# Kernel tuning notes

Hardware: AMD Instinct MI355X
Metric: run time of the kernel (lower is better)

## Reference

```python
import jax, jax.numpy as jnp
import numpy as np

N_HEADS = 16
D_HEAD = 64
N_ROTATE = 32
ROPE_BASE = 10000.0
MAX_LEN = 2048  # round_up_to_multiple_of_256(keep count); static for jit
BATCH, SEQ = 2, 4096


def setup_inputs() -> dict:
    key = jax.random.key(0)
    kq, kk, kv = jax.random.split(key, 3)
    q = jax.random.normal(kq, (BATCH, N_HEADS, MAX_LEN, D_HEAD), jnp.float32)
    k = jax.random.normal(kk, (BATCH, N_HEADS, SEQ, D_HEAD), jnp.float32)
    v = jax.random.normal(kv, (BATCH, N_HEADS, SEQ, D_HEAD), jnp.float32)
    # causal full mask [batch, seq, seq] and full position ids [batch, seq]
    mask_full = jnp.broadcast_to(jnp.tril(jnp.ones((SEQ, SEQ), bool)), (BATCH, SEQ, SEQ))
    pos_full = jnp.broadcast_to(jnp.arange(SEQ, dtype=jnp.int32), (BATCH, SEQ))
    # skip_mask: exactly MAX_LEN kept tokens per row (random positions)
    rng = np.random.default_rng(0)
    sm = np.zeros((BATCH, SEQ), dtype=bool)
    for i in range(BATCH):
        sm[i, rng.permutation(SEQ)[:MAX_LEN]] = True
    return {"q": q, "k": k, "v": v, "mask_full": mask_full,
            "pos_full": pos_full, "skip_mask": jnp.asarray(sm)}


def _rope_rotate(x, pos):
    # x: [b, h, L, n_rotate], pos: [b, L]
    half = N_ROTATE // 2
    inv_freq = 1.0 / (ROPE_BASE ** (jnp.arange(0, N_ROTATE, 2, dtype=jnp.float32) / N_ROTATE))
    freqs = pos.astype(jnp.float32)[..., None] * inv_freq          # [b, L, half]
    emb = jnp.concatenate([freqs, freqs], axis=-1)[:, None]        # [b, 1, L, n_rotate]
    cos, sin = jnp.cos(emb), jnp.sin(emb)
    x1, x2 = x[..., :half], x[..., half:]
    rot = jnp.concatenate([-x2, x1], axis=-1)                      # rotate_half
    return x * cos + rot * sin


def reference(q, k, v, mask_full, pos_full, skip_mask):
    b, S = skip_mask.shape
    lengths = skip_mask.sum(axis=1)
    # vectorized _trim_attention_mask: stable argsort compacts kept indices to the front
    order = jnp.argsort(jnp.where(skip_mask, 0, 1), axis=1, stable=True)
    idx = order[:, :MAX_LEN]                                       # [b, max_len]
    brow = jnp.arange(b)[:, None]
    mask_trim = mask_full[brow, idx]                               # [b, max_len, S]
    pos_trim = pos_full[brow, idx]                                 # [b, max_len]
    valid = jnp.arange(MAX_LEN)[None, :] < lengths[:, None]
    mask_trim = mask_trim & valid[..., None]
    pos_trim = jnp.where(valid, pos_trim, 0)

    # partial RoPE on first n_rotate channels
    rq = _rope_rotate(q[..., :N_ROTATE], pos_trim)
    rk = _rope_rotate(k[..., :N_ROTATE], pos_full)
    q = jnp.concatenate([rq, q[..., N_ROTATE:]], axis=-1)
    k = jnp.concatenate([rk, k[..., N_ROTATE:]], axis=-1)

    # masked SDPA (bool mask broadcast over heads)
    scale = 1.0 / jnp.sqrt(jnp.float32(D_HEAD))
    scores = jnp.einsum('bhqd,bhkd->bhqk', q, k) * scale
    scores = jnp.where(mask_trim[:, None], scores, jnp.finfo(scores.dtype).min)
    attn = jax.nn.softmax(scores, axis=-1)
    return jnp.einsum('bhqk,bhkd->bhqd', attn, v)
```

## Files before the change

kernel.cpp:

```cpp
#include <hip/hip_runtime.h>
#include <math.h>

#define BB 2
#define HH 16
#define QQ 2048
#define SS 4096
#define DD 64
#define NRH 16
#define NQT 32

typedef unsigned short u16;
typedef unsigned int   u32;
typedef short bhalf8 __attribute__((ext_vector_type(8)));
typedef float f32x4  __attribute__((ext_vector_type(4)));

typedef __attribute__((address_space(1))) const u32 gu32;
typedef __attribute__((address_space(3))) u32 lu32;

#if __has_builtin(__builtin_amdgcn_exp2f)
#define EXP2(x) __builtin_amdgcn_exp2f(x)
#else
#define EXP2(x) exp2f(x)
#endif

union Frag16 { uint4 u; bhalf8 v; u16 s[8]; uint2 d[2]; };

__device__ __forceinline__ u16 f2bf(float f) {
  union { float f; u32 u; } c; c.f = f;
  return (u16)((c.u + 0x7FFFu + ((c.u >> 16) & 1u)) >> 16);
}

__device__ __forceinline__ u32 cvt_pk_bf16(float lo, float hi) {
  u32 r;
  asm("v_cvt_pk_bf16_f32 %0, %1, %2" : "=v"(r) : "v"(lo), "v"(hi));
  return r;
}

__device__ __forceinline__ bhalf8 ldfrag(const u16* p) {
  Frag16 f; f.u = *reinterpret_cast<const uint4*>(p); return f.v;
}

__device__ __forceinline__ void rope32(float* x, int pos) {
  const float step = 0.8304820237218405f;
  const float fp = (float)pos;
#pragma unroll
  for (int i = 0; i < NRH; ++i) {
    float ang = fp * exp2f(-step * (float)i);
    float sv, cv;
    __sincosf(ang, &sv, &cv);
    float a = x[i], b = x[i + NRH];
    x[i]       = a * cv - b * sv;
    x[i + NRH] = b * cv + a * sv;
  }
}

__global__ void prep_idx_kernel(const unsigned char* __restrict__ sm,
                                int* __restrict__ idx) {
  __shared__ int wsum[4];
  __shared__ int modes;
  const int tid = threadIdx.x;
  const int b = (int)blockIdx.x;

  int c = 0;
  for (int i = 0; i < 32; ++i) c += (sm[tid * 32 + i] != 0) ? 1 : 0;
#pragma unroll
  for (int off = 32; off; off >>= 1) c += __shfl_down(c, off);
  if ((tid & 63) == 0) wsum[tid >> 6] = c;
  __syncthreads();
  if (tid == 0) modes = (wsum[0] + wsum[1] + wsum[2] + wsum[3] > 3000) ? 1 : 0;
  __syncthreads();
  const bool byteMode = (modes != 0);
  const u32* sm32 = (const u32*)sm;

  const int base = b * SS + tid * 16;
  u32 flags = 0;
  for (int i = 0; i < 16; ++i) {
    bool f = byteMode ? (sm[base + i] != 0) : (sm32[base + i] != 0);
    flags |= ((u32)(f ? 1 : 0)) << i;
  }
  int cnt = __popc(flags);
  int vv = cnt;
#pragma unroll
  for (int off = 1; off < 64; off <<= 1) {
    int t = __shfl_up(vv, off);
    if ((tid & 63) >= off) vv += t;
  }
  __syncthreads();
  if ((tid & 63) == 63) wsum[tid >> 6] = vv;
  __syncthreads();
  int add = 0;
  for (int w2 = 0; w2 < (tid >> 6); ++w2) add += wsum[w2];
  int p = vv - cnt + add;
  for (int i = 0; i < 16; ++i) {
    if (flags & (1u << i)) {
      if (p < QQ) idx[b * QQ + p] = tid * 16 + i;
      ++p;
    }
  }
}

__global__ __launch_bounds__(256) void prep_kv_kernel(const float* __restrict__ k,
                                                      const float* __restrict__ v,
                                                      u16* __restrict__ kbf,
                                                      u16* __restrict__ vt) {
  __shared__ u16 tile[64][72];
  if (blockIdx.x < 512) {
    int r = blockIdx.x * 256 + threadIdx.x;
    int pos = r & (SS - 1);
    float x[64];
    const float4* src = (const float4*)(k + (size_t)r * DD);
#pragma unroll
    for (int i = 0; i < 16; ++i) {
      float4 t = src[i];
      x[4 * i] = t.x; x[4 * i + 1] = t.y; x[4 * i + 2] = t.z; x[4 * i + 3] = t.w;
    }
    rope32(x, pos);
    u16 tmp[64];
#pragma unroll
    for (int i = 0; i < 64; ++i) tmp[i] = f2bf(x[i]);
    uint4* dst = (uint4*)(kbf + (size_t)r * DD);
#pragma unroll
    for (int i = 0; i < 8; ++i) dst[i] = ((uint4*)tmp)[i];
  } else {
    int blk = (int)blockIdx.x - 512;
    int bh = blk >> 6;
    int jt = blk & 63;
    int t = threadIdx.x;
    int jl = t >> 2;
    int dc = (t & 3) * 16;
    const float4* src = (const float4*)(v + ((size_t)(bh * SS + jt * 64 + jl)) * DD + dc);
#pragma unroll
    for (int i = 0; i < 4; ++i) {
      float4 f = src[i];
      tile[jl][dc + 4 * i]     = f2bf(f.x);
      tile[jl][dc + 4 * i + 1] = f2bf(f.y);
      tile[jl][dc + 4 * i + 2] = f2bf(f.z);
      tile[jl][dc + 4 * i + 3] = f2bf(f.w);
    }
    __syncthreads();
    int d = t >> 2;
    int c = t & 3;
    u16 o[16];
#pragma unroll
    for (int m = 0; m < 16; ++m)
      o[m] = tile[4 * c + (m >> 2) + ((m & 3) << 4)][d];
    uint4* dst = (uint4*)(vt + ((size_t)(bh * DD + d)) * SS + jt * 64 + c * 16);
    dst[0] = ((uint4*)o)[0];
    dst[1] = ((uint4*)o)[1];
  }
}

__device__ __forceinline__ void stage_tiles(const char* kb_bh, const char* vt_bh,
                                            u16* Kb, u16* Vb, int t0,
                                            int w, int srow, int schk) {
#pragma unroll
  for (int p2 = 0; p2 < 2; ++p2) {
    const int rr = w * 16 + p2 * 8 + srow;
    {
      const char* g = kb_bh + (size_t)(t0 + rr) * 128 + ((schk ^ (rr & 7)) * 16);
      lu32* l = (lu32*)((char*)Kb + (w * 16 + p2 * 8) * 128);
      __builtin_amdgcn_global_load_lds((gu32*)g, l, 16, 0, 0);
    }
    {
      const char* g = vt_bh + (size_t)rr * (SS * 2) + t0 * 2 + ((schk ^ (rr & 7)) * 16);
      lu32* l = (lu32*)((char*)Vb + (w * 16 + p2 * 8) * 128);
      __builtin_amdgcn_global_load_lds((gu32*)g, l, 16, 0, 0);
    }
  }
}

template <bool MASKED>
__device__ __forceinline__ void attn_tile(
    const u16* __restrict__ Kb, const u16* __restrict__ Vb, u16* __restrict__ pb,
    int t0, int grp, int col,
    int bnd0, int bnd1, int bnd2, int bnd3,
    int paIdx0, int paIdx1,
    int pwIdx0, int pwIdx1, int pwIdx2, int pwIdx3,
    bhalf8 qa0, bhalf8 qa1,
    f32x4& acc0, f32x4& acc1, f32x4& acc2, f32x4& acc3,
    float& l0, float& l1, float& l2, float& l3) {
  const int swz = col & 7;
  f32x4 s0 = {0.f, 0.f, 0.f, 0.f}, s1 = s0, s2 = s0, s3 = s0;
  {
    const u16* kr0 = Kb + (0 * 16 + col) * 64;
    const u16* kr1 = Kb + (1 * 16 + col) * 64;
    const u16* kr2 = Kb + (2 * 16 + col) * 64;
    const u16* kr3 = Kb + (3 * 16 + col) * 64;
    __builtin_amdgcn_s_setprio(1);
    s0 = __builtin_amdgcn_mfma_f32_16x16x32_bf16(qa0, ldfrag(kr0 + ((grp ^ swz) * 8)), s0, 0, 0, 0);
    s1 = __builtin_amdgcn_mfma_f32_16x16x32_bf16(qa0, ldfrag(kr1 + ((grp ^ swz) * 8)), s1, 0, 0, 0);
    s2 = __builtin_amdgcn_mfma_f32_16x16x32_bf16(qa0, ldfrag(kr2 + ((grp ^ swz) * 8)), s2, 0, 0, 0);
    s3 = __builtin_amdgcn_mfma_f32_16x16x32_bf16(qa0, ldfrag(kr3 + ((grp ^ swz) * 8)), s3, 0, 0, 0);
    s0 = __builtin_amdgcn_mfma_f32_16x16x32_bf16(qa1, ldfrag(kr0 + (((4 + grp) ^ swz) * 8)), s0, 0, 0, 0);
    s1 = __builtin_amdgcn_mfma_f32_16x16x32_bf16(qa1, ldfrag(kr1 + (((4 + grp) ^ swz) * 8)), s1, 0, 0, 0);
    s2 = __builtin_amdgcn_mfma_f32_16x16x32_bf16(qa1, ldfrag(kr2 + (((4 + grp) ^ swz) * 8)), s2, 0, 0, 0);
    s3 = __builtin_amdgcn_mfma_f32_16x16x32_bf16(qa1, ldfrag(kr3 + (((4 + grp) ^ swz) * 8)), s3, 0, 0, 0);
    __builtin_amdgcn_s_setprio(0);
  }

  const int key0 = t0 + col;
#define SM_ROW(R, BND, LACC, PWI)                                              \
  {                                                                            \
    float p0, p1, p2v, p3;                                                     \
    if (MASKED) {                                                              \
      p0  = (key0      <= (BND)) ? EXP2(s0[R] - 16.f) : 0.f;                   \
      p1  = (key0 + 16 <= (BND)) ? EXP2(s1[R] - 16.f) : 0.f;                   \
      p2v = (key0 + 32 <= (BND)) ? EXP2(s2[R] - 16.f) : 0.f;                   \
      p3  = (key0 + 48 <= (BND)) ? EXP2(s3[R] - 16.f) : 0.f;                   \
    } else {                                                                   \
      p0  = EXP2(s0[R] - 16.f);                                                \
      p1  = EXP2(s1[R] - 16.f);                                                \
      p2v = EXP2(s2[R] - 16.f);                                                \
      p3  = EXP2(s3[R] - 16.f);                                                \
    }                                                                          \
    (LACC) += (p0 + p1) + (p2v + p3);                                          \
    uint2 pw;                                                                  \
    pw.x = cvt_pk_bf16(p0, p1);                                                \
    pw.y = cvt_pk_bf16(p2v, p3);                                               \
    *(uint2*)(pb + (PWI)) = pw;                                                \
  }
  SM_ROW(0, bnd0, l0, pwIdx0)
  SM_ROW(1, bnd1, l1, pwIdx1)
  SM_ROW(2, bnd2, l2, pwIdx2)
  SM_ROW(3, bnd3, l3, pwIdx3)
#undef SM_ROW

  bhalf8 pa0, pa1;
  {
    Frag16 f0, f1;
    f0.u = *(const uint4*)(pb + paIdx0);
    f1.u = *(const uint4*)(pb + paIdx1);
    pa0 = f0.v; pa1 = f1.v;
  }

  {
    const u16* vr0 = Vb + (0 * 16 + col) * 64;
    const u16* vr1 = Vb + (1 * 16 + col) * 64;
    const u16* vr2 = Vb + (2 * 16 + col) * 64;
    const u16* vr3 = Vb + (3 * 16 + col) * 64;
    __builtin_amdgcn_s_setprio(1);
    acc0 = __builtin_amdgcn_mfma_f32_16x16x32_bf16(pa0, ldfrag(vr0 + ((grp ^ swz) * 8)), acc0, 0, 0, 0);
    acc1 = __builtin_amdgcn_mfma_f32_16x16x32_bf16(pa0, ldfrag(vr1 + ((grp ^ swz) * 8)), acc1, 0, 0, 0);
    acc2 = __builtin_amdgcn_mfma_f32_16x16x32_bf16(pa0, ldfrag(vr2 + ((grp ^ swz) * 8)), acc2, 0, 0, 0);
    acc3 = __builtin_amdgcn_mfma_f32_16x16x32_bf16(pa0, ldfrag(vr3 + ((grp ^ swz) * 8)), acc3, 0, 0, 0);
    acc0 = __builtin_amdgcn_mfma_f32_16x16x32_bf16(pa1, ldfrag(vr0 + (((4 + grp) ^ swz) * 8)), acc0, 0, 0, 0);
    acc1 = __builtin_amdgcn_mfma_f32_16x16x32_bf16(pa1, ldfrag(vr1 + (((4 + grp) ^ swz) * 8)), acc1, 0, 0, 0);
    acc2 = __builtin_amdgcn_mfma_f32_16x16x32_bf16(pa1, ldfrag(vr2 + (((4 + grp) ^ swz) * 8)), acc2, 0, 0, 0);
    acc3 = __builtin_amdgcn_mfma_f32_16x16x32_bf16(pa1, ldfrag(vr3 + (((4 + grp) ^ swz) * 8)), acc3, 0, 0, 0);
    __builtin_amdgcn_s_setprio(0);
  }
}

__global__ __launch_bounds__(256, 4) void attn_mfma_kernel(
    const float* __restrict__ qsrc, const u16* __restrict__ kbf,
    const u16* __restrict__ vt, const int* __restrict__ idx,
    float* __restrict__ out) {
  __shared__ u16 KbufA[64 * 64];
  __shared__ u16 VbufA[64 * 64];
  __shared__ u16 KbufB[64 * 64];
  __shared__ u16 VbufB[64 * 64];
  __shared__ __align__(16) u16 Pbuf[4][16 * 64];

  const int blk = (int)blockIdx.x;
  const int bh  = blk & 31;
  const int qt  = (NQT - 1) - (blk >> 5);
  const int q0  = qt * 64;
  const int b   = bh >> 4;
  const int tid  = threadIdx.x;
  const int w    = tid >> 6;
  const int lane = tid & 63;
  const int grp  = lane >> 4;
  const int col  = lane & 15;

  const char* kb_bh = (const char*)(kbf + (size_t)bh * SS * DD);
  const char* vt_bh = (const char*)(vt + (size_t)bh * DD * SS);

  const int srow = lane >> 3;
  const int schk = lane & 7;

  u16* pb = Pbuf[w];

  const int* idxb = idx + b * QQ + q0;
  const int bnd0 = idxb[w * 16 + grp * 4 + 0];
  const int bnd1 = idxb[w * 16 + grp * 4 + 1];
  const int bnd2 = idxb[w * 16 + grp * 4 + 2];
  const int bnd3 = idxb[w * 16 + grp * 4 + 3];
  const int wave_minb = idxb[w * 16];
  const int wave_maxb = idxb[w * 16 + 15];
  const int maxbound  = idxb[63];
  const int ntiles = (maxbound >> 6) + 1;

  const int paIdx0 = col * 64 + ((grp ^ (col & 7)) << 3);
  const int paIdx1 = col * 64 + (((grp + 4) ^ (col & 7)) << 3);
  const int qg = grp * 4;
  const int pwIdx0 = (qg + 0) * 64 + ((((col >> 1) ^ ((qg + 0) & 7))) << 3) + ((col & 1) << 2);
  const int pwIdx1 = (qg + 1) * 64 + ((((col >> 1) ^ ((qg + 1) & 7))) << 3) + ((col & 1) << 2);
  const int pwIdx2 = (qg + 2) * 64 + ((((col >> 1) ^ ((qg + 2) & 7))) << 3) + ((col & 1) << 2);
  const int pwIdx3 = (qg + 3) * 64 + ((((col >> 1) ^ ((qg + 3) & 7))) << 3) + ((col & 1) << 2);

  bhalf8 qa0, qa1;
  {
    const int qrow = q0 + w * 16 + col;
    const int mypos = idx[b * QQ + qrow];
    const float* qr = qsrc + (size_t)(bh * QQ + qrow) * DD;
    const int lof = (grp & 1) * 8;
    float4 A0 = *(const float4*)(qr + lof);
    float4 A1 = *(const float4*)(qr + lof + 4);
    float4 B0 = *(const float4*)(qr + 16 + lof);
    float4 B1 = *(const float4*)(qr + 16 + lof + 4);
    float4 C0 = *(const float4*)(qr + 32 + grp * 8);
    float4 C1 = *(const float4*)(qr + 32 + grp * 8 + 4);
    float xlo[8] = {A0.x, A0.y, A0.z, A0.w, A1.x, A1.y, A1.z, A1.w};
    float xhi[8] = {B0.x, B0.y, B0.z, B0.w, B1.x, B1.y, B1.z, B1.w};
    float xq1[8] = {C0.x, C0.y, C0.z, C0.w, C1.x, C1.y, C1.z, C1.w};
    const float scq = 0.125f * 1.44269504088896f;
    const float fp = (float)mypos;
    Frag16 f0, f1;
#pragma unroll
    for (int j = 0; j < 8; ++j) {
      float ang = fp * exp2f(-0.8304820237218405f * (float)(lof + j));
      float sv, cv;
      __sincosf(ang, &sv, &cv);
      float val = (grp >= 2) ? (xhi[j] * cv + xlo[j] * sv)
                             : (xlo[j] * cv - xhi[j] * sv);
      f0.s[j] = f2bf(val * scq);
      f1.s[j] = f2bf(xq1[j] * scq);
    }
    qa0 = f0.v; qa1 = f1.v;
  }

  f32x4 acc0 = {0.f, 0.f, 0.f, 0.f}, acc1 = acc0, acc2 = acc0, acc3 = acc0;
  float l0 = 0.f, l1 = 0.f, l2 = 0.f, l3 = 0.f;

  stage_tiles(kb_bh, vt_bh, KbufA, VbufA, 0, w, srow, schk);
  __syncthreads();

  for (int ti = 0; ti < ntiles; ti += 2) {
    const bool has1 = (ti + 1) < ntiles;
    if (has1) stage_tiles(kb_bh, vt_bh, KbufB, VbufB, (ti + 1) << 6, w, srow, schk);
    {
      const int t0 = ti << 6;
      if (t0 <= wave_maxb) {
        if (t0 + 63 <= wave_minb)
          attn_tile<false>(KbufA, VbufA, pb, t0, grp, col, bnd0, bnd1, bnd2, bnd3,
                           paIdx0, paIdx1, pwIdx0, pwIdx1, pwIdx2, pwIdx3,
                           qa0, qa1, acc0, acc1, acc2, acc3, l0, l1, l2, l3);
        else
          attn_tile<true>(KbufA, VbufA, pb, t0, grp, col, bnd0, bnd1, bnd2, bnd3,
                          paIdx0, paIdx1, pwIdx0, pwIdx1, pwIdx2, pwIdx3,
                          qa0, qa1, acc0, acc1, acc2, acc3, l0, l1, l2, l3);
      }
    }
    __syncthreads();
    if (has1) {
      if (ti + 2 < ntiles)
        stage_tiles(kb_bh, vt_bh, KbufA, VbufA, (ti + 2) << 6, w, srow, schk);
      {
        const int t0 = (ti + 1) << 6;
        if (t0 <= wave_maxb) {
          if (t0 + 63 <= wave_minb)
            attn_tile<false>(KbufB, VbufB, pb, t0, grp, col, bnd0, bnd1, bnd2, bnd3,
                             paIdx0, paIdx1, pwIdx0, pwIdx1, pwIdx2, pwIdx3,
                             qa0, qa1, acc0, acc1, acc2, acc3, l0, l1, l2, l3);
          else
            attn_tile<true>(KbufB, VbufB, pb, t0, grp, col, bnd0, bnd1, bnd2, bnd3,
                            paIdx0, paIdx1, pwIdx0, pwIdx1, pwIdx2, pwIdx3,
                            qa0, qa1, acc0, acc1, acc2, acc3, l0, l1, l2, l3);
        }
      }
      __syncthreads();
    }
  }

#pragma unroll
  for (int mdel = 1; mdel < 16; mdel <<= 1) {
    l0 += __shfl_xor(l0, mdel);
    l1 += __shfl_xor(l1, mdel);
    l2 += __shfl_xor(l2, mdel);
    l3 += __shfl_xor(l3, mdel);
  }
  float i0 = 1.f / l0, i1 = 1.f / l1, i2 = 1.f / l2, i3 = 1.f / l3;
  float* ob = out + (size_t)(bh * QQ + q0 + w * 16 + grp * 4) * DD + col;
#pragma unroll
  for (int r = 0; r < 4; ++r) {
    float iv = (r == 0) ? i0 : (r == 1) ? i1 : (r == 2) ? i2 : i3;
    ob[(size_t)r * DD + 0]  = acc0[r] * iv;
    ob[(size_t)r * DD + 16] = acc1[r] * iv;
    ob[(size_t)r * DD + 32] = acc2[r] * iv;
    ob[(size_t)r * DD + 48] = acc3[r] * iv;
  }
}

__global__ __launch_bounds__(64) void attn_fb_kernel(const float* __restrict__ q,
                                                     const float* __restrict__ ksrc,
                                                     const float* __restrict__ v,
                                                     const int* __restrict__ idx,
                                                     float* __restrict__ out) {
  int t = (int)(gridDim.x - 1u - blockIdx.x);
  int sub = t >> 5;
  int bh = t & 31;
  int b = bh >> 4;
  int lane = threadIdx.x;
  int qi = sub * 64 + lane;
  const int bound = idx[b * QQ + qi];

  float qreg[64];
  {
    const float4* qp = (const float4*)(q + ((size_t)bh * QQ + qi) * DD);
#pragma unroll
    for (int i = 0; i < 16; ++i) {
      float4 t4 = qp[i];
      qreg[4 * i] = t4.x; qreg[4 * i + 1] = t4.y;
      qreg[4 * i + 2] = t4.z; qreg[4 * i + 3] = t4.w;
    }
  }
  rope32(qreg, bound);
#pragma unroll
  for (int i = 0; i < 64; ++i) qreg[i] *= 0.125f;

  const float* kbase = ksrc + (size_t)bh * SS * DD;
  const float* vbase = v + (size_t)bh * SS * DD;
  float acc[64];
#pragma unroll
  for (int i = 0; i < 64; ++i) acc[i] = 0.f;
  float mrun = -INFINITY, lrun = 0.f;

  for (int j = 0; j <= bound; ++j) {
    float ka[64];
    const float4* kp = (const float4*)(kbase + (size_t)j * DD);
#pragma unroll
    for (int i = 0; i < 16; ++i) {
      float4 t4 = kp[i];
      ka[4 * i] = t4.x; ka[4 * i + 1] = t4.y;
      ka[4 * i + 2] = t4.z; ka[4 * i + 3] = t4.w;
    }
    rope32(ka, j);
    float s0 = 0.f, s1 = 0.f, s2 = 0.f, s3 = 0.f;
#pragma unroll
    for (int i = 0; i < 16; ++i) {
      s0 = fmaf(qreg[4 * i], ka[4 * i], s0);
      s1 = fmaf(qreg[4 * i + 1], ka[4 * i + 1], s1);
      s2 = fmaf(qreg[4 * i + 2], ka[4 * i + 2], s2);
      s3 = fmaf(qreg[4 * i + 3], ka[4 * i + 3], s3);
    }
    float sc = (s0 + s1) + (s2 + s3);
    if (sc > mrun) {
      float alpha = __expf(mrun - sc);
      lrun *= alpha;
#pragma unroll
      for (int i = 0; i < 64; ++i) acc[i] *= alpha;
      mrun = sc;
    }
    float pw = __expf(sc - mrun);
    lrun += pw;
    const float4* vp = (const float4*)(vbase + (size_t)j * DD);
#pragma unroll
    for (int i = 0; i < 16; ++i) {
      float4 t4 = vp[i];
      acc[4 * i] = fmaf(pw, t4.x, acc[4 * i]);
      acc[4 * i + 1] = fmaf(pw, t4.y, acc[4 * i + 1]);
      acc[4 * i + 2] = fmaf(pw, t4.z, acc[4 * i + 2]);
      acc[4 * i + 3] = fmaf(pw, t4.w, acc[4 * i + 3]);
    }
  }
  float inv = 1.0f / lrun;
  float4* op = (float4*)(out + ((size_t)bh * QQ + qi) * DD);
#pragma unroll
  for (int i = 0; i < 16; ++i) {
    float4 t4;
    t4.x = acc[4 * i] * inv; t4.y = acc[4 * i + 1] * inv;
    t4.z = acc[4 * i + 2] * inv; t4.w = acc[4 * i + 3] * inv;
    op[i] = t4;
  }
}

extern "C" void kernel_launch(void* const* d_in, const int* in_sizes, int n_in,
                              void* d_out, int out_size, void* d_ws, size_t ws_size,
                              hipStream_t stream) {
  (void)in_sizes; (void)n_in; (void)out_size;
  const float* q = (const float*)d_in[0];
  const float* k = (const float*)d_in[1];
  const float* v = (const float*)d_in[2];
  const unsigned char* skip = (const unsigned char*)d_in[5];
  float* out = (float*)d_out;

  char* base = (char*)d_ws;
  int* idx = (int*)base;
  const size_t kbytes = (size_t)BB * HH * SS * DD * 2;
  u16* kbf = (u16*)(base + 16384);
  u16* vtb = (u16*)(base + 16384 + kbytes);
  const size_t need = 16384 + 2 * kbytes;

  prep_idx_kernel<<<2, 256, 0, stream>>>(skip, idx);
  if (ws_size >= need) {
    prep_kv_kernel<<<512 + BB * HH * 64, 256, 0, stream>>>(k, v, kbf, vtb);
    attn_mfma_kernel<<<NQT * 32, 256, 0, stream>>>(q, kbf, vtb, idx, out);
  } else {
    attn_fb_kernel<<<1024, 64, 0, stream>>>(q, k, v, idx, out);
  }
}
```

Before: 296.8 us.

## Compute transposed S and O tiles to keep P in registers, dropping LDS round-trip

Swaps the MFMA operand order so each lane holds scores for one query row across four consecutive keys. The bf16 P fragment can then be packed straight from registers into the PV MFMA operand instead of being written to and read back from a per-wave shared-memory buffer. The V transpose kernel permutes key order to match the new fragment layout. The row-sum reduction shrinks to two shuffles, the mask bound becomes a single per-lane value, and output stores become float4 writes. The risk is that any mismatch between the permuted V layout and the P register packing gives silently wrong results.

```diff
diff --git a/kernel.cpp b/kernel.cpp
--- a/kernel.cpp
+++ b/kernel.cpp
@@ -142,8 +142,11 @@
     int c = t & 3;
     u16 o[16];
 #pragma unroll
-    for (int m = 0; m < 16; ++m)
-      o[m] = tile[4 * c + (m >> 2) + ((m & 3) << 4)][d];
+    for (int m = 0; m < 16; ++m) {
+      int p = c * 16 + m;
+      int kp = (p & 32) | ((p & 4) << 2) | ((p >> 1) & 12) | (p & 3);
+      o[m] = tile[kp][d];
+    }
     uint4* dst = (uint4*)(vt + ((size_t)(bh * DD + d)) * SS + jt * 64 + c * 16);
     dst[0] = ((uint4*)o)[0];
     dst[1] = ((uint4*)o)[1];
@@ -171,82 +174,95 @@
 
 template <bool MASKED>
 __device__ __forceinline__ void attn_tile(
-    const u16* __restrict__ Kb, const u16* __restrict__ Vb, u16* __restrict__ pb,
-    int t0, int grp, int col,
-    int bnd0, int bnd1, int bnd2, int bnd3,
-    int paIdx0, int paIdx1,
-    int pwIdx0, int pwIdx1, int pwIdx2, int pwIdx3,
+    const u16* __restrict__ Kb, const u16* __restrict__ Vb,
+    int t0, int grp, int col, int bnd,
     bhalf8 qa0, bhalf8 qa1,
     f32x4& acc0, f32x4& acc1, f32x4& acc2, f32x4& acc3,
-    float& l0, float& l1, float& l2, float& l3) {
+    float& lsum) {
   const int swz = col & 7;
-  f32x4 s0 = {0.f, 0.f, 0.f, 0.f}, s1 = s0, s2 = s0, s3 = s0;
+  f32x4 z = {0.f, 0.f, 0.f, 0.f};
+  f32x4 s0 = z, s1 = z, s2 = z, s3 = z;
   {
     const u16* kr0 = Kb + (0 * 16 + col) * 64;
     const u16* kr1 = Kb + (1 * 16 + col) * 64;
     const u16* kr2 = Kb + (2 * 16 + col) * 64;
     const u16* kr3 = Kb + (3 * 16 + col) * 64;
     __builtin_amdgcn_s_setprio(1);
-    s0 = __builtin_amdgcn_mfma_f32_16x16x32_bf16(qa0, ldfrag(kr0 + ((grp ^ swz) * 8)), s0, 0, 0, 0);
-    s1 = __builtin_amdgcn_mfma_f32_16x16x32_bf16(qa0, ldfrag(kr1 + ((grp ^ swz) * 8)), s1, 0, 0, 0);
-    s2 = __builtin_amdgcn_mfma_f32_16x16x32_bf16(qa0, ldfrag(kr2 + ((grp ^ swz) * 8)), s2, 0, 0, 0);
-    s3 = __builtin_amdgcn_mfma_f32_16x16x32_bf16(qa0, ldfrag(kr3 + ((grp ^ swz) * 8)), s3, 0, 0, 0);
-    s0 = __builtin_amdgcn_mfma_f32_16x16x32_bf16(qa1, ldfrag(kr0 + (((4 + grp) ^ swz) * 8)), s0, 0, 0, 0);
-    s1 = __builtin_amdgcn_mfma_f32_16x16x32_bf16(qa1, ldfrag(kr1 + (((4 + grp) ^ swz) * 8)), s1, 0, 0, 0);
-    s2 = __builtin_amdgcn_mfma_f32_16x16x32_bf16(qa1, ldfrag(kr2 + (((4 + grp) ^ swz) * 8)), s2, 0, 0, 0);
-    s3 = __builtin_amdgcn_mfma_f32_16x16x32_bf16(qa1, ldfrag(kr3 + (((4 + grp) ^ swz) * 8)), s3, 0, 0, 0);
+    bhalf8 a0 = ldfrag(kr0 + ((grp ^ swz) * 8));
+    s0 = __builtin_amdgcn_mfma_f32_16x16x32_bf16(a0, qa0, s0, 0, 0, 0);
+    bhalf8 b0 = ldfrag(kr0 + (((4 + grp) ^ swz) * 8));
+    s0 = __builtin_amdgcn_mfma_f32_16x16x32_bf16(b0, qa1, s0, 0, 0, 0);
+    bhalf8 a1 = ldfrag(kr1 + ((grp ^ swz) * 8));
+    s1 = __builtin_amdgcn_mfma_f32_16x16x32_bf16(a1, qa0, s1, 0, 0, 0);
+    bhalf8 b1 = ldfrag(kr1 + (((4 + grp) ^ swz) * 8));
+    s1 = __builtin_amdgcn_mfma_f32_16x16x32_bf16(b1, qa1, s1, 0, 0, 0);
+    bhalf8 a2 = ldfrag(kr2 + ((grp ^ swz) * 8));
+    s2 = __builtin_amdgcn_mfma_f32_16x16x32_bf16(a2, qa0, s2, 0, 0, 0);
+    bhalf8 b2 = ldfrag(kr2 + (((4 + grp) ^ swz) * 8));
+    s2 = __builtin_amdgcn_mfma_f32_16x16x32_bf16(b2, qa1, s2, 0, 0, 0);
+    bhalf8 a3 = ldfrag(kr3 + ((grp ^ swz) * 8));
+    s3 = __builtin_amdgcn_mfma_f32_16x16x32_bf16(a3, qa0, s3, 0, 0, 0);
+    bhalf8 b3 = ldfrag(kr3 + (((4 + grp) ^ swz) * 8));
+    s3 = __builtin_amdgcn_mfma_f32_16x16x32_bf16(b3, qa1, s3, 0, 0, 0);
     __builtin_amdgcn_s_setprio(0);
   }
 
-  const int key0 = t0 + col;
-#define SM_ROW(R, BND, LACC, PWI)                                              \
+  uint2 w0, w1, w2, w3;
+#define SM_C(SC, CB, W)                                                        \
   {                                                                            \
     float p0, p1, p2v, p3;                                                     \
+    const int kb = t0 + (CB) + grp * 4;                                        \
     if (MASKED) {                                                              \
-      p0  = (key0      <= (BND)) ? EXP2(s0[R] - 16.f) : 0.f;                   \
-      p1  = (key0 + 16 <= (BND)) ? EXP2(s1[R] - 16.f) : 0.f;                   \
-      p2v = (key0 + 32 <= (BND)) ? EXP2(s2[R] - 16.f) : 0.f;                   \
-      p3  = (key0 + 48 <= (BND)) ? EXP2(s3[R] - 16.f) : 0.f;                   \
+      p0  = (kb + 0 <= bnd) ? EXP2(SC[0] - 16.f) : 0.f;                        \
+      p1  = (kb + 1 <= bnd) ? EXP2(SC[1] - 16.f) : 0.f;                        \
+      p2v = (kb + 2 <= bnd) ? EXP2(SC[2] - 16.f) : 0.f;                        \
+      p3  = (kb + 3 <= bnd) ? EXP2(SC[3] - 16.f) : 0.f;                        \
     } else {                                                                   \
-      p0  = EXP2(s0[R] - 16.f);                                                \
-      p1  = EXP2(s1[R] - 16.f);                                                \
-      p2v = EXP2(s2[R] - 16.f);                                                \
-      p3  = EXP2(s3[R] - 16.f);                                                \
+      p0  = EXP2(SC[0] - 16.f);                                                \
+      p1  = EXP2(SC[1] - 16.f);                                                \
+      p2v = EXP2(SC[2] - 16.f);                                                \
+      p3  = EXP2(SC[3] - 16.f);                                                \
     }                                                                          \
-    (LACC) += (p0 + p1) + (p2v + p3);                                          \
-    uint2 pw;                                                                  \
-    pw.x = cvt_pk_bf16(p0, p1);                                                \
-    pw.y = cvt_pk_bf16(p2v, p3);                                               \
-    *(uint2*)(pb + (PWI)) = pw;                                                \
-  }
-  SM_ROW(0, bnd0, l0, pwIdx0)
-  SM_ROW(1, bnd1, l1, pwIdx1)
-  SM_ROW(2, bnd2, l2, pwIdx2)
-  SM_ROW(3, bnd3, l3, pwIdx3)
-#undef SM_ROW
-
-  bhalf8 pa0, pa1;
+    lsum += (p0 + p1) + (p2v + p3);                                            \
+    W.x = cvt_pk_bf16(p0, p1);                                                 \
+    W.y = cvt_pk_bf16(p2v, p3);                                                \
+  }
+  SM_C(s0, 0,  w0)
+  SM_C(s1, 16, w1)
+  SM_C(s2, 32, w2)
+  SM_C(s3, 48, w3)
+#undef SM_C
+
+  bhalf8 pv0, pv1;
   {
     Frag16 f0, f1;
-    f0.u = *(const uint4*)(pb + paIdx0);
-    f1.u = *(const uint4*)(pb + paIdx1);
-    pa0 = f0.v; pa1 = f1.v;
-  }
-
-  {
-    const u16* vr0 = Vb + (0 * 16 + col) * 64;
-    const u16* vr1 = Vb + (1 * 16 + col) * 64;
-    const u16* vr2 = Vb + (2 * 16 + col) * 64;
-    const u16* vr3 = Vb + (3 * 16 + col) * 64;
+    f0.d[0] = w0; f0.d[1] = w1;
+    f1.d[0] = w2; f1.d[1] = w3;
+    pv0 = f0.v; pv1 = f1.v;
+  }
+
+  {
+    const u16* vr0 = Vb + (0  + col) * 64;
+    const u16* vr1 = Vb + (16 + col) * 64;
+    const u16* vr2 = Vb + (32 + col) * 64;
+    const u16* vr3 = Vb + (48 + col) * 64;
     __builtin_amdgcn_s_setprio(1);
-    acc0 = __builtin_amdgcn_mfma_f32_16x16x32_bf16(pa0, ldfrag(vr0 + ((grp ^ swz) * 8)), acc0, 0, 0, 0);
-    acc1 = __builtin_amdgcn_mfma_f32_16x16x32_bf16(pa0, ldfrag(vr1 + ((grp ^ swz) * 8)), acc1, 0, 0, 0);
-    acc2 = __builtin_amdgcn_mfma_f32_16x16x32_bf16(pa0, ldfrag(vr2 + ((grp ^ swz) * 8)), acc2, 0, 0, 0);
-    acc3 = __builtin_amdgcn_mfma_f32_16x16x32_bf16(pa0, ldfrag(vr3 + ((grp ^ swz) * 8)), acc3, 0, 0, 0);
-    acc0 = __builtin_amdgcn_mfma_f32_16x16x32_bf16(pa1, ldfrag(vr0 + (((4 + grp) ^ swz) * 8)), acc0, 0, 0, 0);
-    acc1 = __builtin_amdgcn_mfma_f32_16x16x32_bf16(pa1, ldfrag(vr1 + (((4 + grp) ^ swz) * 8)), acc1, 0, 0, 0);
-    acc2 = __builtin_amdgcn_mfma_f32_16x16x32_bf16(pa1, ldfrag(vr2 + (((4 + grp) ^ swz) * 8)), acc2, 0, 0, 0);
-    acc3 = __builtin_amdgcn_mfma_f32_16x16x32_bf16(pa1, ldfrag(vr3 + (((4 + grp) ^ swz) * 8)), acc3, 0, 0, 0);
+    bhalf8 x0 = ldfrag(vr0 + ((grp ^ swz) * 8));
+    acc0 = __builtin_amdgcn_mfma_f32_16x16x32_bf16(x0, pv0, acc0, 0, 0, 0);
+    bhalf8 y0 = ldfrag(vr0 + (((4 + grp) ^ swz) * 8));
+    acc0 = __builtin_amdgcn_mfma_f32_16x16x32_bf16(y0, pv1, acc0, 0, 0, 0);
+    bhalf8 x1 = ldfrag(vr1 + ((grp ^ swz) * 8));
+    acc1 = __builtin_amdgcn_mfma_f32_16x16x32_bf16(x1, pv0, acc1, 0, 0, 0);
+    bhalf8 y1 = ldfrag(vr1 + (((4 + grp) ^ swz) * 8));
+    acc1 = __builtin_amdgcn_mfma_f32_16x16x32_bf16(y1, pv1, acc1, 0, 0, 0);
+    bhalf8 x2 = ldfrag(vr2 + ((grp ^ swz) * 8));
+    acc2 = __builtin_amdgcn_mfma_f32_16x16x32_bf16(x2, pv0, acc2, 0, 0, 0);
+    bhalf8 y2 = ldfrag(vr2 + (((4 + grp) ^ swz) * 8));
+    acc2 = __builtin_amdgcn_mfma_f32_16x16x32_bf16(y2, pv1, acc2, 0, 0, 0);
+    bhalf8 x3 = ldfrag(vr3 + ((grp ^ swz) * 8));
+    acc3 = __builtin_amdgcn_mfma_f32_16x16x32_bf16(x3, pv0, acc3, 0, 0, 0);
+    bhalf8 y3 = ldfrag(vr3 + (((4 + grp) ^ swz) * 8));
+    acc3 = __builtin_amdgcn_mfma_f32_16x16x32_bf16(y3, pv1, acc3, 0, 0, 0);
     __builtin_amdgcn_s_setprio(0);
   }
 }
@@ -259,7 +275,6 @@
   __shared__ u16 VbufA[64 * 64];
   __shared__ u16 KbufB[64 * 64];
   __shared__ u16 VbufB[64 * 64];
-  __shared__ __align__(16) u16 Pbuf[4][16 * 64];
 
   const int blk = (int)blockIdx.x;
   const int bh  = blk & 31;
@@ -278,30 +293,16 @@
   const int srow = lane >> 3;
   const int schk = lane & 7;
 
-  u16* pb = Pbuf[w];
-
   const int* idxb = idx + b * QQ + q0;
-  const int bnd0 = idxb[w * 16 + grp * 4 + 0];
-  const int bnd1 = idxb[w * 16 + grp * 4 + 1];
-  const int bnd2 = idxb[w * 16 + grp * 4 + 2];
-  const int bnd3 = idxb[w * 16 + grp * 4 + 3];
+  const int bnd = idxb[w * 16 + col];
   const int wave_minb = idxb[w * 16];
   const int wave_maxb = idxb[w * 16 + 15];
   const int maxbound  = idxb[63];
   const int ntiles = (maxbound >> 6) + 1;
 
-  const int paIdx0 = col * 64 + ((grp ^ (col & 7)) << 3);
-  const int paIdx1 = col * 64 + (((grp + 4) ^ (col & 7)) << 3);
-  const int qg = grp * 4;
-  const int pwIdx0 = (qg + 0) * 64 + ((((col >> 1) ^ ((qg + 0) & 7))) << 3) + ((col & 1) << 2);
-  const int pwIdx1 = (qg + 1) * 64 + ((((col >> 1) ^ ((qg + 1) & 7))) << 3) + ((col & 1) << 2);
-  const int pwIdx2 = (qg + 2) * 64 + ((((col >> 1) ^ ((qg + 2) & 7))) << 3) + ((col & 1) << 2);
-  const int pwIdx3 = (qg + 3) * 64 + ((((col >> 1) ^ ((qg + 3) & 7))) << 3) + ((col & 1) << 2);
-
   bhalf8 qa0, qa1;
   {
     const int qrow = q0 + w * 16 + col;
-    const int mypos = idx[b * QQ + qrow];
     const float* qr = qsrc + (size_t)(bh * QQ + qrow) * DD;
     const int lof = (grp & 1) * 8;
     float4 A0 = *(const float4*)(qr + lof);
@@ -314,7 +315,7 @@
     float xhi[8] = {B0.x, B0.y, B0.z, B0.w, B1.x, B1.y, B1.z, B1.w};
     float xq1[8] = {C0.x, C0.y, C0.z, C0.w, C1.x, C1.y, C1.z, C1.w};
     const float scq = 0.125f * 1.44269504088896f;
-    const float fp = (float)mypos;
+    const float fp = (float)bnd;
     Frag16 f0, f1;
 #pragma unroll
     for (int j = 0; j < 8; ++j) {
@@ -329,8 +330,12 @@
     qa0 = f0.v; qa1 = f1.v;
   }
 
-  f32x4 acc0 = {0.f, 0.f, 0.f, 0.f}, acc1 = acc0, acc2 = acc0, acc3 = acc0;
-  float l0 = 0.f, l1 = 0.f, l2 = 0.f, l3 = 0.f;
+  f32x4 z = {0.f, 0.f, 0.f, 0.f};
+  f32x4 acc0 = z, acc1 = z, acc2 = z, acc3 = z;
+  float lsum = 0.f;
+
+#define ATTN_CALL(M, KB, VB, T0)                                               \
+  attn_tile<M>(KB, VB, T0, grp, col, bnd, qa0, qa1, acc0, acc1, acc2, acc3, lsum)
 
   stage_tiles(kb_bh, vt_bh, KbufA, VbufA, 0, w, srow, schk);
   __syncthreads();
@@ -341,14 +346,8 @@
     {
       const int t0 = ti << 6;
       if (t0 <= wave_maxb) {
-        if (t0 + 63 <= wave_minb)
-          attn_tile<false>(KbufA, VbufA, pb, t0, grp, col, bnd0, bnd1, bnd2, bnd3,
-                           paIdx0, paIdx1, pwIdx0, pwIdx1, pwIdx2, pwIdx3,
-                           qa0, qa1, acc0, acc1, acc2, acc3, l0, l1, l2, l3);
-        else
-          attn_tile<true>(KbufA, VbufA, pb, t0, grp, col, bnd0, bnd1, bnd2, bnd3,
-                          paIdx0, paIdx1, pwIdx0, pwIdx1, pwIdx2, pwIdx3,
-                          qa0, qa1, acc0, acc1, acc2, acc3, l0, l1, l2, l3);
+        if (t0 + 63 <= wave_minb) ATTN_CALL(false, KbufA, VbufA, t0);
+        else                      ATTN_CALL(true,  KbufA, VbufA, t0);
       }
     }
     __syncthreads();
@@ -358,36 +357,29 @@
       {
         const int t0 = (ti + 1) << 6;
         if (t0 <= wave_maxb) {
-          if (t0 + 63 <= wave_minb)
-            attn_tile<false>(KbufB, VbufB, pb, t0, grp, col, bnd0, bnd1, bnd2, bnd3,
-                             paIdx0, paIdx1, pwIdx0, pwIdx1, pwIdx2, pwIdx3,
-                             qa0, qa1, acc0, acc1, acc2, acc3, l0, l1, l2, l3);
-          else
-            attn_tile<true>(KbufB, VbufB, pb, t0, grp, col, bnd0, bnd1, bnd2, bnd3,
-                            paIdx0, paIdx1, pwIdx0, pwIdx1, pwIdx2, pwIdx3,
-                            qa0, qa1, acc0, acc1, acc2, acc3, l0, l1, l2, l3);
+          if (t0 + 63 <= wave_minb) ATTN_CALL(false, KbufB, VbufB, t0);
+          else                      ATTN_CALL(true,  KbufB, VbufB, t0);
         }
       }
       __syncthreads();
     }
   }
-
-#pragma unroll
-  for (int mdel = 1; mdel < 16; mdel <<= 1) {
-    l0 += __shfl_xor(l0, mdel);
-    l1 += __shfl_xor(l1, mdel);
-    l2 += __shfl_xor(l2, mdel);
-    l3 += __shfl_xor(l3, mdel);
-  }
-  float i0 = 1.f / l0, i1 = 1.f / l1, i2 = 1.f / l2, i3 = 1.f / l3;
-  float* ob = out + (size_t)(bh * QQ + q0 + w * 16 + grp * 4) * DD + col;
-#pragma unroll
-  for (int r = 0; r < 4; ++r) {
-    float iv = (r == 0) ? i0 : (r == 1) ? i1 : (r == 2) ? i2 : i3;
-    ob[(size_t)r * DD + 0]  = acc0[r] * iv;
-    ob[(size_t)r * DD + 16] = acc1[r] * iv;
-    ob[(size_t)r * DD + 32] = acc2[r] * iv;
-    ob[(size_t)r * DD + 48] = acc3[r] * iv;
+#undef ATTN_CALL
+
+  lsum += __shfl_xor(lsum, 16);
+  lsum += __shfl_xor(lsum, 32);
+  const float inv = 1.f / lsum;
+  float* ob = out + (size_t)(bh * QQ + q0 + w * 16 + col) * DD + grp * 4;
+  {
+    float4 t;
+    t.x = acc0[0] * inv; t.y = acc0[1] * inv; t.z = acc0[2] * inv; t.w = acc0[3] * inv;
+    *(float4*)(ob + 0) = t;
+    t.x = acc1[0] * inv; t.y = acc1[1] * inv; t.z = acc1[2] * inv; t.w = acc1[3] * inv;
+    *(float4*)(ob + 16) = t;
+    t.x = acc2[0] * inv; t.y = acc2[1] * inv; t.z = acc2[2] * inv; t.w = acc2[3] * inv;
+    *(float4*)(ob + 32) = t;
+    t.x = acc3[0] * inv; t.y = acc3[1] * inv; t.z = acc3[2] * inv; t.w = acc3[3] * inv;
+    *(float4*)(ob + 48) = t;
   }
 }
 
```

Result: faster. 288.4 us (-2.8%).
